# Kernel tuning notes

Hardware: AMD Instinct MI355X
Metric: run time of the kernel (lower is better)

The kernel has to match this reference:

```python
import jax, jax.numpy as jnp
import numpy as np

B, T, N, D = 8, 64, 128, 128  # batch, timesteps, num_nodes, hidden_dim
LN_EPS = 1e-5
L2_EPS = 1e-12


def setup_inputs() -> dict:
    key = jax.random.key(0)
    ks = jax.random.split(key, 8)
    feat = jax.random.normal(ks[0], (B, T, N, D), dtype=jnp.float32)
    w = jax.random.uniform(ks[1], (D,), dtype=jnp.float32)  # learned adj gate (torch.rand init)
    s = 1.0 / np.sqrt(D)
    W1 = jax.random.uniform(ks[2], (D, D), dtype=jnp.float32, minval=-s, maxval=s)
    b1 = jax.random.uniform(ks[3], (D,), dtype=jnp.float32, minval=-s, maxval=s)
    W2 = jax.random.uniform(ks[4], (D, D), dtype=jnp.float32, minval=-s, maxval=s)
    b2 = jax.random.uniform(ks[5], (D,), dtype=jnp.float32, minval=-s, maxval=s)
    gamma = jnp.ones((D,), dtype=jnp.float32)
    beta = jnp.zeros((D,), dtype=jnp.float32)
    return {"feat": feat, "w": w, "W1": W1, "b1": b1, "W2": W2, "b2": b2,
            "gamma": gamma, "beta": beta}


def _windows(x):
    # x: (B, T, N, D) -> (B, T-2, 3*N, D): 3 consecutive timesteps flattened over nodes
    b, t, n, d = x.shape
    return jnp.stack([x[:, i:i + t - 2] for i in range(3)], axis=2).reshape(b, t - 2, 3 * n, d)


def reference(feat, w, W1, b1, W2, b2, gamma, beta):
    # gated + L2-normalized features for learned adjacency
    wf = feat * jax.nn.sigmoid(w)
    wf = wf / jnp.maximum(jnp.linalg.norm(wf, axis=-1, keepdims=True), L2_EPS)

    win = _windows(feat)   # (B, T-2, 3N, D)
    wwin = _windows(wf)    # (B, T-2, 3N, D)

    # learned adjacency: gram matrix per window, (B, T-2, 3N, 3N)
    adj = jnp.einsum('btmd,btnd->btmn', wwin, wwin)

    # symmetric normalization D^{-1/2} A D^{-1/2}; inf/nan (deg<=0) -> 0 as in torch
    deg = adj.sum(axis=-1, keepdims=True)
    dis = jnp.where(deg > 0, jax.lax.rsqrt(jnp.maximum(deg, 1e-38)), 0.0)
    nadj = dis * adj * jnp.swapaxes(dis, -1, -2)

    # message passing, keep last N rows (current timestep)
    agg = jnp.einsum('btmn,btnd->btmd', nadj, win)[:, :, -N:, :]

    # FFN (dropout is identity in eval): Linear -> ReLU -> Linear
    h = jax.nn.relu(agg @ W1 + b1) @ W2 + b2

    # residual with current-timestep features + LayerNorm
    s = feat[:, 2:] + h
    mu = s.mean(axis=-1, keepdims=True)
    var = ((s - mu) ** 2).mean(axis=-1, keepdims=True)
    return (s - mu) * jax.lax.rsqrt(var + LN_EPS) * gamma + beta
```

## Files before the change

### kernel.cpp

```cpp
#include <hip/hip_runtime.h>
#include <math.h>

#define BB    8
#define TDIM  64
#define NN    128
#define DD    128
#define TTOUT 62
#define W3    384
#define LG    136
#define LP    40
#define LW    72

typedef __attribute__((ext_vector_type(8))) short bf16x8;
typedef __attribute__((ext_vector_type(4))) float f32x4;

__device__ __forceinline__ float sigf(float x){ return 1.0f/(1.0f+__expf(-x)); }
__device__ __forceinline__ unsigned short f2bf(float x){
  union{float f; unsigned u;} v; v.f=x;
  unsigned r = v.u + 0x7FFFu + ((v.u>>16)&1u);
  return (unsigned short)(r>>16);
}

__global__ __launch_bounds__(512) void k_pre(const float* __restrict__ feat,
    const float* __restrict__ w, const float* __restrict__ W1, const float* __restrict__ W2,
    float* __restrict__ rscale, float* __restrict__ ssum,
    unsigned short* __restrict__ W1T, unsigned short* __restrict__ W2T){
  __shared__ float sSig[DD];
  __shared__ float sPart[8*DD];
  const int bid = blockIdx.x, tid = threadIdx.x;
  if(bid >= BB*TDIM){
    const float* W = (bid == BB*TDIM) ? W1 : W2;
    unsigned short* WT = (bid == BB*TDIM) ? W1T : W2T;
    for(int e=tid; e<DD*DD; e+=512){
      int k = e>>7, n = e&127;
      WT[n*DD + k] = f2bf(W[(size_t)k*DD + n]);
    }
    return;
  }
  const int bt = bid;
  if(tid < DD) sSig[tid] = sigf(w[tid]);
  __syncthreads();
  const int row = tid >> 2, q = tid & 3;
  const float* fp = feat + ((size_t)bt*NN + row)*DD + q*32;
  float g[32];
  #pragma unroll
  for(int i=0;i<8;i++){
    float4 v = *(const float4*)(fp + i*4);
    g[i*4]=v.x; g[i*4+1]=v.y; g[i*4+2]=v.z; g[i*4+3]=v.w;
  }
  float ss = 0.f;
  #pragma unroll
  for(int j=0;j<32;j++){ g[j] *= sSig[q*32+j]; ss += g[j]*g[j]; }
  ss += __shfl_xor(ss,1); ss += __shfl_xor(ss,2);
  float rs = 1.0f / fmaxf(sqrtf(ss), 1e-12f);
  if(q==0) rscale[(size_t)bt*NN + row] = rs;
  #pragma unroll
  for(int j=0;j<32;j++) g[j] *= rs;
  #pragma unroll
  for(int k=4;k<64;k<<=1){
    #pragma unroll
    for(int j=0;j<32;j++) g[j] += __shfl_xor(g[j], k);
  }
  const int lane = tid & 63, wid = tid >> 6;
  if((lane>>2)==0){
    #pragma unroll
    for(int j=0;j<32;j++) sPart[wid*DD + q*32 + j] = g[j];
  }
  __syncthreads();
  if(tid < DD){
    float s = 0.f;
    #pragma unroll
    for(int wv=0; wv<8; wv++) s += sPart[wv*DD + tid];
    ssum[(size_t)bt*DD + tid] = s;
  }
}

__global__ void k_dis(const float* __restrict__ feat, const float* __restrict__ w,
                      const float* __restrict__ rscale, const float* __restrict__ ssum,
                      float* __restrict__ dis){
  __shared__ float s3[DD];
  __shared__ float sg[DD];
  int bt2 = blockIdx.x;
  int b = bt2 / TTOUT, tt = bt2 % TTOUT;
  int tid = threadIdx.x;
  if(tid < DD){
    int base = (b*TDIM + tt)*DD;
    s3[tid] = ssum[base+tid] + ssum[base+DD+tid] + ssum[base+2*DD+tid];
    sg[tid] = sigf(w[tid]);
  }
  __syncthreads();
  int gr = (b*TDIM + tt)*NN + tid;
  const float4* fr = (const float4*)(feat + (size_t)gr*DD);
  float deg = 0.f;
  #pragma unroll 8
  for(int q=0;q<DD/4;q++){
    float4 f = fr[q];
    deg += f.x*sg[q*4+0]*s3[q*4+0] + f.y*sg[q*4+1]*s3[q*4+1]
         + f.z*sg[q*4+2]*s3[q*4+2] + f.w*sg[q*4+3]*s3[q*4+3];
  }
  deg *= rscale[gr];
  dis[(size_t)bt2*W3 + tid] = (deg > 0.f) ? rsqrtf(fmaxf(deg, 1e-38f)) : 0.f;
}

__global__ __launch_bounds__(512,4) void k_main(
    const float* __restrict__ feat,
    const float* __restrict__ w,
    const float* __restrict__ rscale, const float* __restrict__ dis,
    const unsigned short* __restrict__ W1T, const float* __restrict__ b1,
    const unsigned short* __restrict__ W2T, const float* __restrict__ b2,
    const float* __restrict__ gamma, const float* __restrict__ beta,
    float* __restrict__ out)
{
  __shared__ __align__(16) unsigned short sm[32000];
  __shared__ float sSig[DD];
  unsigned short* sA  = sm;
  unsigned short* sG  = sm + 17408;
  unsigned short* sFt = sm + 21760;
  unsigned short* sP  = sm + 26880;
  unsigned short* sWt = sm + 17408;

  const int tid = threadIdx.x;
  const int bid = blockIdx.x;
  const int bt2 = (bid & 7)*62 + (bid >> 3);
  const int rowBase = (bt2/TTOUT)*TDIM*NN + (bt2%TTOUT)*NN;
  const float* disP = dis + (size_t)bt2*W3;

  const int lane = tid & 63, wid = tid >> 6;
  const int l15 = lane & 15, l4 = lane >> 4;
  const int m0 = wid * 16;

  if(tid < DD) sSig[tid] = sigf(w[tid]);
  __syncthreads();

  #pragma unroll
  for(int e0=0; e0<8; ++e0){
    int e = e0*512 + tid;
    int d = e & 127, r0 = (e>>7)*4;
    float sg = sSig[d];
    #pragma unroll
    for(int i=0;i<4;i++){
      int j = 256 + r0 + i, gr = rowBase + j;
      float f = feat[(size_t)gr*DD + d];
      float fac = rscale[gr]*disP[j];
      sA[(r0+i)*LG + d] = f2bf(f*sg*fac);
    }
  }

  f32x4 acc2[8];
  #pragma unroll
  for(int i=0;i<8;i++) acc2[i] = (f32x4){0.f,0.f,0.f,0.f};

  for(int c=0; c<12; ++c){
    const int n0 = c*32;
    __syncthreads();
    #pragma unroll
    for(int e0=0; e0<2; ++e0){
      int e = e0*512 + tid;
      int d = e & 127, r0 = (e>>7)*4;
      float sg = sSig[d];
      unsigned short fb[4];
      #pragma unroll
      for(int i=0;i<4;i++){
        int j = n0 + r0 + i, gr = rowBase + j;
        float f = feat[(size_t)gr*DD + d];
        float fac = rscale[gr]*disP[j];
        fb[i] = f2bf(f);
        sG[(r0+i)*LG + d] = f2bf(f*sg*fac);
      }
      unsigned int* fp = (unsigned int*)&sFt[d*LP + r0];
      fp[0] = (unsigned)fb[0] | ((unsigned)fb[1]<<16);
      fp[1] = (unsigned)fb[2] | ((unsigned)fb[3]<<16);
    }
    __syncthreads();

    f32x4 p0 = {0.f,0.f,0.f,0.f}, p1 = {0.f,0.f,0.f,0.f};
    #pragma unroll
    for(int ks=0; ks<4; ++ks){
      bf16x8 aA  = *(const bf16x8*)&sA[(m0+l15)*LG + ks*32 + l4*8];
      bf16x8 bg0 = *(const bf16x8*)&sG[( 0+l15)*LG + ks*32 + l4*8];
      bf16x8 bg1 = *(const bf16x8*)&sG[(16+l15)*LG + ks*32 + l4*8];
      p0 = __builtin_amdgcn_mfma_f32_16x16x32_bf16(aA, bg0, p0, 0,0,0);
      p1 = __builtin_amdgcn_mfma_f32_16x16x32_bf16(aA, bg1, p1, 0,0,0);
    }
    #pragma unroll
    for(int r=0;r<4;r++){
      sP[(m0 + l4*4 + r)*LP +  0 + l15] = f2bf(p0[r]);
      sP[(m0 + l4*4 + r)*LP + 16 + l15] = f2bf(p1[r]);
    }
    __syncthreads();

    bf16x8 aP = *(const bf16x8*)&sP[(m0+l15)*LP + l4*8];
    #pragma unroll
    for(int dt=0; dt<8; ++dt){
      bf16x8 bF = *(const bf16x8*)&sFt[(dt*16+l15)*LP + l4*8];
      acc2[dt] = __builtin_amdgcn_mfma_f32_16x16x32_bf16(aP, bF, acc2[dt], 0,0,0);
    }
  }

  #pragma unroll
  for(int dt=0; dt<8; ++dt)
    #pragma unroll
    for(int r=0;r<4;r++)
      sA[(m0+l4*4+r)*LG + dt*16+l15] = f2bf(acc2[dt][r]);

  f32x4 acch[8];
  #pragma unroll
  for(int dt=0; dt<8; ++dt){
    float bv = b1[dt*16+l15];
    acch[dt] = (f32x4){bv,bv,bv,bv};
  }
  for(int kh=0; kh<2; ++kh){
    __syncthreads();
    #pragma unroll
    for(int it=0; it<2; ++it){
      int e = it*512 + tid, n = e>>3, sg2 = e&7;
      uint4 v = *(const uint4*)(W1T + (size_t)n*DD + kh*64 + sg2*8);
      *(uint4*)(sWt + n*LW + sg2*8) = v;
    }
    __syncthreads();
    #pragma unroll
    for(int ks=0; ks<2; ++ks){
      bf16x8 aA = *(const bf16x8*)&sA[(m0+l15)*LG + kh*64 + ks*32 + l4*8];
      #pragma unroll
      for(int dt=0; dt<8; ++dt){
        bf16x8 bW = *(const bf16x8*)&sWt[(dt*16+l15)*LW + ks*32 + l4*8];
        acch[dt] = __builtin_amdgcn_mfma_f32_16x16x32_bf16(aA, bW, acch[dt], 0,0,0);
      }
    }
  }
  __syncthreads();
  #pragma unroll
  for(int dt=0; dt<8; ++dt)
    #pragma unroll
    for(int r=0;r<4;r++)
      sA[(m0+l4*4+r)*LG + dt*16+l15] = f2bf(fmaxf(acch[dt][r], 0.f));

  f32x4 acco[8];
  #pragma unroll
  for(int dt=0; dt<8; ++dt){
    float bv = b2[dt*16+l15];
    acco[dt] = (f32x4){bv,bv,bv,bv};
  }
  for(int kh=0; kh<2; ++kh){
    __syncthreads();
    #pragma unroll
    for(int it=0; it<2; ++it){
      int e = it*512 + tid, n = e>>3, sg2 = e&7;
      uint4 v = *(const uint4*)(W2T + (size_t)n*DD + kh*64 + sg2*8);
      *(uint4*)(sWt + n*LW + sg2*8) = v;
    }
    __syncthreads();
    #pragma unroll
    for(int ks=0; ks<2; ++ks){
      bf16x8 aA = *(const bf16x8*)&sA[(m0+l15)*LG + kh*64 + ks*32 + l4*8];
      #pragma unroll
      for(int dt=0; dt<8; ++dt){
        bf16x8 bW = *(const bf16x8*)&sWt[(dt*16+l15)*LW + ks*32 + l4*8];
        acco[dt] = __builtin_amdgcn_mfma_f32_16x16x32_bf16(aA, bW, acco[dt], 0,0,0);
      }
    }
  }

  const float* fres = feat + (size_t)(rowBase + 256)*DD;
  #pragma unroll
  for(int r=0;r<4;r++){
    int m = m0 + l4*4 + r;
    float vals[8]; float s1 = 0.f, s2 = 0.f;
    #pragma unroll
    for(int dt=0; dt<8; ++dt){
      int d = dt*16 + l15;
      float v = acco[dt][r] + fres[(size_t)m*DD + d];
      vals[dt] = v; s1 += v; s2 += v*v;
    }
    #pragma unroll
    for(int k=1;k<16;k<<=1){ s1 += __shfl_xor(s1,k); s2 += __shfl_xor(s2,k); }
    float mu   = s1*(1.0f/DD);
    float rstd = rsqrtf(s2*(1.0f/DD) - mu*mu + 1e-5f);
    #pragma unroll
    for(int dt=0; dt<8; ++dt){
      int d = dt*16 + l15;
      out[((size_t)bt2*NN + m)*DD + d] = (vals[dt]-mu)*rstd*gamma[d] + beta[d];
    }
  }
}

extern "C" void kernel_launch(void* const* d_in, const int* in_sizes, int n_in,
                              void* d_out, int out_size, void* d_ws, size_t ws_size,
                              hipStream_t stream){
  const float* feat  = (const float*)d_in[0];
  const float* w     = (const float*)d_in[1];
  const float* W1    = (const float*)d_in[2];
  const float* b1    = (const float*)d_in[3];
  const float* W2    = (const float*)d_in[4];
  const float* b2    = (const float*)d_in[5];
  const float* gamma = (const float*)d_in[6];
  const float* beta  = (const float*)d_in[7];
  float* out = (float*)d_out;

  char* ws = (char*)d_ws;
  float* rscale = (float*)(ws + 0);
  float* ssum   = (float*)(ws + 262144);
  float* dis    = (float*)(ws + 524288);
  unsigned short* W1T = (unsigned short*)(ws + 1286144);
  unsigned short* W2T = (unsigned short*)(ws + 1318912);

  k_pre<<<BB*TDIM + 2, 512, 0, stream>>>(feat, w, W1, W2, rscale, ssum, W1T, W2T);
  k_dis<<<BB*TTOUT, W3, 0, stream>>>(feat, w, rscale, ssum, dis);
  k_main<<<BB*TTOUT, 512, 0, stream>>>(feat, w, rscale, dis, W1T, b1, W2T, b2,
                                       gamma, beta, out);
}
```

Measured before the change: 89.82 us.

## Swizzle shared-memory tiles, restructure column-sum in k_pre, remap k_dis blocks

Replaces the padded shared-memory strides in k_main with XOR-swizzled layouts for the A, G, transposed-feature, P and weight tiles. The aim is to avoid LDS bank conflicts without padding, at the cost of a slightly larger LDS footprint. k_pre now computes the per-timestep column sum with a direct strided loop over rows weighted by the row scale, instead of a 32-register xor-shuffle butterfly. This is meant to cut shuffle work and register pressure. k_dis also adopts the same interleaved block-to-window mapping as k_main.

```diff
diff --git a/kernel.cpp b/kernel.cpp
--- a/kernel.cpp
+++ b/kernel.cpp
@@ -7,9 +7,6 @@
 #define DD    128
 #define TTOUT 62
 #define W3    384
-#define LG    136
-#define LP    40
-#define LW    72
 
 typedef __attribute__((ext_vector_type(8))) short bf16x8;
 typedef __attribute__((ext_vector_type(4))) float f32x4;
@@ -20,13 +17,16 @@
   unsigned r = v.u + 0x7FFFu + ((v.u>>16)&1u);
   return (unsigned short)(r>>16);
 }
+__device__ __forceinline__ int swzA(int row, int col){ return row*128 + (col ^ ((row&7)<<3)); }
+__device__ __forceinline__ int swzF(int row, int col){ return row*64  + (col ^ ((row&7)<<3)); }
 
 __global__ __launch_bounds__(512) void k_pre(const float* __restrict__ feat,
     const float* __restrict__ w, const float* __restrict__ W1, const float* __restrict__ W2,
     float* __restrict__ rscale, float* __restrict__ ssum,
     unsigned short* __restrict__ W1T, unsigned short* __restrict__ W2T){
   __shared__ float sSig[DD];
-  __shared__ float sPart[8*DD];
+  __shared__ float sRs[NN];
+  __shared__ float sPart[4*DD];
   const int bid = blockIdx.x, tid = threadIdx.x;
   if(bid >= BB*TDIM){
     const float* W = (bid == BB*TDIM) ? W1 : W2;
@@ -42,37 +42,28 @@
   __syncthreads();
   const int row = tid >> 2, q = tid & 3;
   const float* fp = feat + ((size_t)bt*NN + row)*DD + q*32;
-  float g[32];
+  float ss = 0.f;
   #pragma unroll
   for(int i=0;i<8;i++){
     float4 v = *(const float4*)(fp + i*4);
-    g[i*4]=v.x; g[i*4+1]=v.y; g[i*4+2]=v.z; g[i*4+3]=v.w;
-  }
-  float ss = 0.f;
-  #pragma unroll
-  for(int j=0;j<32;j++){ g[j] *= sSig[q*32+j]; ss += g[j]*g[j]; }
+    float g0 = v.x*sSig[q*32+i*4+0], g1 = v.y*sSig[q*32+i*4+1];
+    float g2 = v.z*sSig[q*32+i*4+2], g3 = v.w*sSig[q*32+i*4+3];
+    ss += g0*g0 + g1*g1 + g2*g2 + g3*g3;
+  }
   ss += __shfl_xor(ss,1); ss += __shfl_xor(ss,2);
   float rs = 1.0f / fmaxf(sqrtf(ss), 1e-12f);
-  if(q==0) rscale[(size_t)bt*NN + row] = rs;
-  #pragma unroll
-  for(int j=0;j<32;j++) g[j] *= rs;
-  #pragma unroll
-  for(int k=4;k<64;k<<=1){
-    #pragma unroll
-    for(int j=0;j<32;j++) g[j] += __shfl_xor(g[j], k);
-  }
-  const int lane = tid & 63, wid = tid >> 6;
-  if((lane>>2)==0){
-    #pragma unroll
-    for(int j=0;j<32;j++) sPart[wid*DD + q*32 + j] = g[j];
-  }
-  __syncthreads();
-  if(tid < DD){
-    float s = 0.f;
-    #pragma unroll
-    for(int wv=0; wv<8; wv++) s += sPart[wv*DD + tid];
-    ssum[(size_t)bt*DD + tid] = s;
-  }
+  if(q==0){ rscale[(size_t)bt*NN + row] = rs; sRs[row] = rs; }
+  __syncthreads();
+  const int d = tid & 127, rg = tid >> 7;
+  const float* fc = feat + ((size_t)bt*NN + rg*32)*DD + d;
+  float acc = 0.f;
+  #pragma unroll 8
+  for(int i=0;i<32;i++) acc += fc[(size_t)i*DD] * sRs[rg*32+i];
+  sPart[rg*DD + d] = acc;
+  __syncthreads();
+  if(tid < DD)
+    ssum[(size_t)bt*DD + tid] =
+      (sPart[tid] + sPart[DD+tid] + sPart[2*DD+tid] + sPart[3*DD+tid]) * sSig[tid];
 }
 
 __global__ void k_dis(const float* __restrict__ feat, const float* __restrict__ w,
@@ -80,7 +71,7 @@
                       float* __restrict__ dis){
   __shared__ float s3[DD];
   __shared__ float sg[DD];
-  int bt2 = blockIdx.x;
+  int bt2 = (blockIdx.x & 7)*62 + (blockIdx.x >> 3);
   int b = bt2 / TTOUT, tt = bt2 % TTOUT;
   int tid = threadIdx.x;
   if(tid < DD){
@@ -111,13 +102,13 @@
     const float* __restrict__ gamma, const float* __restrict__ beta,
     float* __restrict__ out)
 {
-  __shared__ __align__(16) unsigned short sm[32000];
+  __shared__ __align__(16) unsigned short sm[36864];
   __shared__ float sSig[DD];
   unsigned short* sA  = sm;
-  unsigned short* sG  = sm + 17408;
-  unsigned short* sFt = sm + 21760;
-  unsigned short* sP  = sm + 26880;
-  unsigned short* sWt = sm + 17408;
+  unsigned short* sG  = sm + 16384;
+  unsigned short* sFt = sm + 20480;
+  unsigned short* sP  = sm + 28672;
+  unsigned short* sWt = sm + 16384;
 
   const int tid = threadIdx.x;
   const int bid = blockIdx.x;
@@ -142,7 +133,7 @@
       int j = 256 + r0 + i, gr = rowBase + j;
       float f = feat[(size_t)gr*DD + d];
       float fac = rscale[gr]*disP[j];
-      sA[(r0+i)*LG + d] = f2bf(f*sg*fac);
+      sA[swzA(r0+i, d)] = f2bf(f*sg*fac);
     }
   }
 
@@ -165,9 +156,9 @@
         float f = feat[(size_t)gr*DD + d];
         float fac = rscale[gr]*disP[j];
         fb[i] = f2bf(f);
-        sG[(r0+i)*LG + d] = f2bf(f*sg*fac);
+        sG[swzA(r0+i, d)] = f2bf(f*sg*fac);
       }
-      unsigned int* fp = (unsigned int*)&sFt[d*LP + r0];
+      unsigned int* fp = (unsigned int*)&sFt[swzF(d, r0)];
       fp[0] = (unsigned)fb[0] | ((unsigned)fb[1]<<16);
       fp[1] = (unsigned)fb[2] | ((unsigned)fb[3]<<16);
     }
@@ -176,32 +167,33 @@
     f32x4 p0 = {0.f,0.f,0.f,0.f}, p1 = {0.f,0.f,0.f,0.f};
     #pragma unroll
     for(int ks=0; ks<4; ++ks){
-      bf16x8 aA  = *(const bf16x8*)&sA[(m0+l15)*LG + ks*32 + l4*8];
-      bf16x8 bg0 = *(const bf16x8*)&sG[( 0+l15)*LG + ks*32 + l4*8];
-      bf16x8 bg1 = *(const bf16x8*)&sG[(16+l15)*LG + ks*32 + l4*8];
+      bf16x8 aA  = *(const bf16x8*)&sA[swzA(m0+l15, ks*32 + l4*8)];
+      bf16x8 bg0 = *(const bf16x8*)&sG[swzA( 0+l15, ks*32 + l4*8)];
+      bf16x8 bg1 = *(const bf16x8*)&sG[swzA(16+l15, ks*32 + l4*8)];
       p0 = __builtin_amdgcn_mfma_f32_16x16x32_bf16(aA, bg0, p0, 0,0,0);
       p1 = __builtin_amdgcn_mfma_f32_16x16x32_bf16(aA, bg1, p1, 0,0,0);
     }
     #pragma unroll
     for(int r=0;r<4;r++){
-      sP[(m0 + l4*4 + r)*LP +  0 + l15] = f2bf(p0[r]);
-      sP[(m0 + l4*4 + r)*LP + 16 + l15] = f2bf(p1[r]);
-    }
-    __syncthreads();
-
-    bf16x8 aP = *(const bf16x8*)&sP[(m0+l15)*LP + l4*8];
+      sP[swzF(m0 + l4*4 + r,  0 + l15)] = f2bf(p0[r]);
+      sP[swzF(m0 + l4*4 + r, 16 + l15)] = f2bf(p1[r]);
+    }
+    __syncthreads();
+
+    bf16x8 aP = *(const bf16x8*)&sP[swzF(m0+l15, l4*8)];
     #pragma unroll
     for(int dt=0; dt<8; ++dt){
-      bf16x8 bF = *(const bf16x8*)&sFt[(dt*16+l15)*LP + l4*8];
+      bf16x8 bF = *(const bf16x8*)&sFt[swzF(dt*16+l15, l4*8)];
       acc2[dt] = __builtin_amdgcn_mfma_f32_16x16x32_bf16(aP, bF, acc2[dt], 0,0,0);
     }
   }
 
+  unsigned short* ovl = sA;
   #pragma unroll
   for(int dt=0; dt<8; ++dt)
     #pragma unroll
     for(int r=0;r<4;r++)
-      sA[(m0+l4*4+r)*LG + dt*16+l15] = f2bf(acc2[dt][r]);
+      ovl[swzA(m0+l4*4+r, dt*16+l15)] = f2bf(acc2[dt][r]);
 
   f32x4 acch[8];
   #pragma unroll
@@ -215,15 +207,15 @@
     for(int it=0; it<2; ++it){
       int e = it*512 + tid, n = e>>3, sg2 = e&7;
       uint4 v = *(const uint4*)(W1T + (size_t)n*DD + kh*64 + sg2*8);
-      *(uint4*)(sWt + n*LW + sg2*8) = v;
+      *(uint4*)&sWt[swzF(n, sg2*8)] = v;
     }
     __syncthreads();
     #pragma unroll
     for(int ks=0; ks<2; ++ks){
-      bf16x8 aA = *(const bf16x8*)&sA[(m0+l15)*LG + kh*64 + ks*32 + l4*8];
+      bf16x8 aA = *(const bf16x8*)&ovl[swzA(m0+l15, kh*64 + ks*32 + l4*8)];
       #pragma unroll
       for(int dt=0; dt<8; ++dt){
-        bf16x8 bW = *(const bf16x8*)&sWt[(dt*16+l15)*LW + ks*32 + l4*8];
+        bf16x8 bW = *(const bf16x8*)&sWt[swzF(dt*16+l15, ks*32 + l4*8)];
         acch[dt] = __builtin_amdgcn_mfma_f32_16x16x32_bf16(aA, bW, acch[dt], 0,0,0);
       }
     }
@@ -233,7 +225,7 @@
   for(int dt=0; dt<8; ++dt)
     #pragma unroll
     for(int r=0;r<4;r++)
-      sA[(m0+l4*4+r)*LG + dt*16+l15] = f2bf(fmaxf(acch[dt][r], 0.f));
+      ovl[swzA(m0+l4*4+r, dt*16+l15)] = f2bf(fmaxf(acch[dt][r], 0.f));
 
   f32x4 acco[8];
   #pragma unroll
@@ -247,15 +239,15 @@
     for(int it=0; it<2; ++it){
       int e = it*512 + tid, n = e>>3, sg2 = e&7;
       uint4 v = *(const uint4*)(W2T + (size_t)n*DD + kh*64 + sg2*8);
-      *(uint4*)(sWt + n*LW + sg2*8) = v;
+      *(uint4*)&sWt[swzF(n, sg2*8)] = v;
     }
     __syncthreads();
     #pragma unroll
     for(int ks=0; ks<2; ++ks){
-      bf16x8 aA = *(const bf16x8*)&sA[(m0+l15)*LG + kh*64 + ks*32 + l4*8];
+      bf16x8 aA = *(const bf16x8*)&ovl[swzA(m0+l15, kh*64 + ks*32 + l4*8)];
       #pragma unroll
       for(int dt=0; dt<8; ++dt){
-        bf16x8 bW = *(const bf16x8*)&sWt[(dt*16+l15)*LW + ks*32 + l4*8];
+        bf16x8 bW = *(const bf16x8*)&sWt[swzF(dt*16+l15, ks*32 + l4*8)];
         acco[dt] = __builtin_amdgcn_mfma_f32_16x16x32_bf16(aA, bW, acco[dt], 0,0,0);
       }
     }
```

Result: slower. 98.63 us (+9.8%).

## Fuse degree computation into main kernel and drop separate dis kernel

Applied to the files above, without the earlier changes.

Removes the k_dis launch and its global dis buffer. Each k_main block now sums the three ssum slices, computes degrees for all 384 window rows with quad shuffles, and caches a combined rscale*dis factor in LDS. k_pre computes its column sums with strided per-column loads weighted by an LDS copy of rscale, replacing the 32-register shuffle tree. A barrier after the sP store is dropped, since each wave reads back only its own rows. In exchange, k_main does extra feat reads and work in its prologue, and the unfused path no longer exists.

```diff
diff --git a/kernel.cpp b/kernel.cpp
--- a/kernel.cpp
+++ b/kernel.cpp
@@ -26,7 +26,8 @@
     float* __restrict__ rscale, float* __restrict__ ssum,
     unsigned short* __restrict__ W1T, unsigned short* __restrict__ W2T){
   __shared__ float sSig[DD];
-  __shared__ float sPart[8*DD];
+  __shared__ float sRs[NN];
+  __shared__ float sPart[4*DD];
   const int bid = blockIdx.x, tid = threadIdx.x;
   if(bid >= BB*TDIM){
     const float* W = (bid == BB*TDIM) ? W1 : W2;
@@ -42,70 +43,34 @@
   __syncthreads();
   const int row = tid >> 2, q = tid & 3;
   const float* fp = feat + ((size_t)bt*NN + row)*DD + q*32;
-  float g[32];
+  float ss = 0.f;
   #pragma unroll
   for(int i=0;i<8;i++){
     float4 v = *(const float4*)(fp + i*4);
-    g[i*4]=v.x; g[i*4+1]=v.y; g[i*4+2]=v.z; g[i*4+3]=v.w;
-  }
-  float ss = 0.f;
-  #pragma unroll
-  for(int j=0;j<32;j++){ g[j] *= sSig[q*32+j]; ss += g[j]*g[j]; }
+    float g0 = v.x*sSig[q*32+i*4+0], g1 = v.y*sSig[q*32+i*4+1];
+    float g2 = v.z*sSig[q*32+i*4+2], g3 = v.w*sSig[q*32+i*4+3];
+    ss += g0*g0 + g1*g1 + g2*g2 + g3*g3;
+  }
   ss += __shfl_xor(ss,1); ss += __shfl_xor(ss,2);
   float rs = 1.0f / fmaxf(sqrtf(ss), 1e-12f);
-  if(q==0) rscale[(size_t)bt*NN + row] = rs;
-  #pragma unroll
-  for(int j=0;j<32;j++) g[j] *= rs;
-  #pragma unroll
-  for(int k=4;k<64;k<<=1){
-    #pragma unroll
-    for(int j=0;j<32;j++) g[j] += __shfl_xor(g[j], k);
-  }
-  const int lane = tid & 63, wid = tid >> 6;
-  if((lane>>2)==0){
-    #pragma unroll
-    for(int j=0;j<32;j++) sPart[wid*DD + q*32 + j] = g[j];
-  }
-  __syncthreads();
-  if(tid < DD){
-    float s = 0.f;
-    #pragma unroll
-    for(int wv=0; wv<8; wv++) s += sPart[wv*DD + tid];
-    ssum[(size_t)bt*DD + tid] = s;
-  }
-}
-
-__global__ void k_dis(const float* __restrict__ feat, const float* __restrict__ w,
-                      const float* __restrict__ rscale, const float* __restrict__ ssum,
-                      float* __restrict__ dis){
-  __shared__ float s3[DD];
-  __shared__ float sg[DD];
-  int bt2 = blockIdx.x;
-  int b = bt2 / TTOUT, tt = bt2 % TTOUT;
-  int tid = threadIdx.x;
-  if(tid < DD){
-    int base = (b*TDIM + tt)*DD;
-    s3[tid] = ssum[base+tid] + ssum[base+DD+tid] + ssum[base+2*DD+tid];
-    sg[tid] = sigf(w[tid]);
-  }
-  __syncthreads();
-  int gr = (b*TDIM + tt)*NN + tid;
-  const float4* fr = (const float4*)(feat + (size_t)gr*DD);
-  float deg = 0.f;
+  if(q==0){ rscale[(size_t)bt*NN + row] = rs; sRs[row] = rs; }
+  __syncthreads();
+  const int d = tid & 127, rg = tid >> 7;
+  const float* fc = feat + ((size_t)bt*NN + rg*32)*DD + d;
+  float acc = 0.f;
   #pragma unroll 8
-  for(int q=0;q<DD/4;q++){
-    float4 f = fr[q];
-    deg += f.x*sg[q*4+0]*s3[q*4+0] + f.y*sg[q*4+1]*s3[q*4+1]
-         + f.z*sg[q*4+2]*s3[q*4+2] + f.w*sg[q*4+3]*s3[q*4+3];
-  }
-  deg *= rscale[gr];
-  dis[(size_t)bt2*W3 + tid] = (deg > 0.f) ? rsqrtf(fmaxf(deg, 1e-38f)) : 0.f;
+  for(int i=0;i<32;i++) acc += fc[(size_t)i*DD] * sRs[rg*32+i];
+  sPart[rg*DD + d] = acc;
+  __syncthreads();
+  if(tid < DD)
+    ssum[(size_t)bt*DD + tid] =
+      (sPart[tid] + sPart[DD+tid] + sPart[2*DD+tid] + sPart[3*DD+tid]) * sSig[tid];
 }
 
 __global__ __launch_bounds__(512,4) void k_main(
     const float* __restrict__ feat,
     const float* __restrict__ w,
-    const float* __restrict__ rscale, const float* __restrict__ dis,
+    const float* __restrict__ rscale, const float* __restrict__ ssum,
     const unsigned short* __restrict__ W1T, const float* __restrict__ b1,
     const unsigned short* __restrict__ W2T, const float* __restrict__ b2,
     const float* __restrict__ gamma, const float* __restrict__ beta,
@@ -113,6 +78,8 @@
 {
   __shared__ __align__(16) unsigned short sm[32000];
   __shared__ float sSig[DD];
+  __shared__ float s3c[DD];
+  __shared__ float sFac[W3];
   unsigned short* sA  = sm;
   unsigned short* sG  = sm + 17408;
   unsigned short* sFt = sm + 21760;
@@ -122,14 +89,41 @@
   const int tid = threadIdx.x;
   const int bid = blockIdx.x;
   const int bt2 = (bid & 7)*62 + (bid >> 3);
-  const int rowBase = (bt2/TTOUT)*TDIM*NN + (bt2%TTOUT)*NN;
-  const float* disP = dis + (size_t)bt2*W3;
+  const int btIdx = (bt2/TTOUT)*TDIM + (bt2%TTOUT);
+  const int rowBase = btIdx * NN;
 
   const int lane = tid & 63, wid = tid >> 6;
   const int l15 = lane & 15, l4 = lane >> 4;
   const int m0 = wid * 16;
 
-  if(tid < DD) sSig[tid] = sigf(w[tid]);
+  if(tid < DD){
+    float sg = sigf(w[tid]);
+    sSig[tid] = sg;
+    float s3 = ssum[(size_t)btIdx*DD + tid] + ssum[(size_t)(btIdx+1)*DD + tid]
+             + ssum[(size_t)(btIdx+2)*DD + tid];
+    s3c[tid] = s3 * sg;
+  }
+  __syncthreads();
+
+  #pragma unroll
+  for(int rg=0; rg<3; ++rg){
+    int row = rg*128 + (tid>>2), q = tid&3;
+    const float* fpr = feat + (size_t)(rowBase+row)*DD + q*32;
+    float a = 0.f;
+    #pragma unroll
+    for(int i=0;i<8;i++){
+      float4 v = *(const float4*)(fpr + i*4);
+      const float* sc = s3c + q*32 + i*4;
+      a += v.x*sc[0] + v.y*sc[1] + v.z*sc[2] + v.w*sc[3];
+    }
+    a += __shfl_xor(a,1); a += __shfl_xor(a,2);
+    if(q==0){
+      float rs = rscale[rowBase+row];
+      float deg = a * rs;
+      float dis = (deg > 0.f) ? rsqrtf(fmaxf(deg, 1e-38f)) : 0.f;
+      sFac[row] = dis * rs;
+    }
+  }
   __syncthreads();
 
   #pragma unroll
@@ -139,10 +133,9 @@
     float sg = sSig[d];
     #pragma unroll
     for(int i=0;i<4;i++){
-      int j = 256 + r0 + i, gr = rowBase + j;
-      float f = feat[(size_t)gr*DD + d];
-      float fac = rscale[gr]*disP[j];
-      sA[(r0+i)*LG + d] = f2bf(f*sg*fac);
+      int j = 256 + r0 + i;
+      float f = feat[(size_t)(rowBase+j)*DD + d];
+      sA[(r0+i)*LG + d] = f2bf(f*sg*sFac[j]);
     }
   }
 
@@ -161,11 +154,10 @@
       unsigned short fb[4];
       #pragma unroll
       for(int i=0;i<4;i++){
-        int j = n0 + r0 + i, gr = rowBase + j;
-        float f = feat[(size_t)gr*DD + d];
-        float fac = rscale[gr]*disP[j];
+        int j = n0 + r0 + i;
+        float f = feat[(size_t)(rowBase+j)*DD + d];
         fb[i] = f2bf(f);
-        sG[(r0+i)*LG + d] = f2bf(f*sg*fac);
+        sG[(r0+i)*LG + d] = f2bf(f*sg*sFac[j]);
       }
       unsigned int* fp = (unsigned int*)&sFt[d*LP + r0];
       fp[0] = (unsigned)fb[0] | ((unsigned)fb[1]<<16);
@@ -187,7 +179,6 @@
       sP[(m0 + l4*4 + r)*LP +  0 + l15] = f2bf(p0[r]);
       sP[(m0 + l4*4 + r)*LP + 16 + l15] = f2bf(p1[r]);
     }
-    __syncthreads();
 
     bf16x8 aP = *(const bf16x8*)&sP[(m0+l15)*LP + l4*8];
     #pragma unroll
@@ -215,7 +206,7 @@
     for(int it=0; it<2; ++it){
       int e = it*512 + tid, n = e>>3, sg2 = e&7;
       uint4 v = *(const uint4*)(W1T + (size_t)n*DD + kh*64 + sg2*8);
-      *(uint4*)(sWt + n*LW + sg2*8) = v;
+      *(uint4*)&sWt[n*LW + sg2*8] = v;
     }
     __syncthreads();
     #pragma unroll
@@ -247,7 +238,7 @@
     for(int it=0; it<2; ++it){
       int e = it*512 + tid, n = e>>3, sg2 = e&7;
       uint4 v = *(const uint4*)(W2T + (size_t)n*DD + kh*64 + sg2*8);
-      *(uint4*)(sWt + n*LW + sg2*8) = v;
+      *(uint4*)&sWt[n*LW + sg2*8] = v;
     }
     __syncthreads();
     #pragma unroll
@@ -300,12 +291,10 @@
   char* ws = (char*)d_ws;
   float* rscale = (float*)(ws + 0);
   float* ssum   = (float*)(ws + 262144);
-  float* dis    = (float*)(ws + 524288);
-  unsigned short* W1T = (unsigned short*)(ws + 1286144);
-  unsigned short* W2T = (unsigned short*)(ws + 1318912);
+  unsigned short* W1T = (unsigned short*)(ws + 524288);
+  unsigned short* W2T = (unsigned short*)(ws + 557056);
 
   k_pre<<<BB*TDIM + 2, 512, 0, stream>>>(feat, w, W1, W2, rscale, ssum, W1T, W2T);
-  k_dis<<<BB*TTOUT, W3, 0, stream>>>(feat, w, rscale, ssum, dis);
-  k_main<<<BB*TTOUT, 512, 0, stream>>>(feat, w, rscale, dis, W1T, b1, W2T, b2,
+  k_main<<<BB*TTOUT, 512, 0, stream>>>(feat, w, rscale, ssum, W1T, b1, W2T, b2,
                                        gamma, beta, out);
 }
```

Result: faster. 81.36 us (-9.4%).
